# Kernel tuning notes

Measured on AMD Instinct MI355X. Metric: run time of the kernel, lower is better.

Reference implementation:

```python
import jax, jax.numpy as jnp
import numpy as np

JITTER = 1e-6
ND = 20       # num_draws
STEPS = 10    # num_steps
G = 100       # num_gammas: PG truncation terms
NUM_CLASSES = 2


def _rbf(X, outputscale, lengthscale):
    x2 = jnp.sum(X * X, axis=-1)
    d2 = jnp.maximum(x2[:, None] + x2[None, :] - 2.0 * (X @ X.T), 0.0)
    return outputscale * jnp.exp(-0.5 * d2 / (lengthscale * lengthscale))


def _chol(K):
    return jnp.linalg.cholesky(K + JITTER * jnp.eye(K.shape[-1], dtype=K.dtype))


def _pg_draw(key, c):
    # PG(1, c) via truncated infinite gamma convolution (G terms):
    # omega = (1/(2 pi^2)) * sum_k Exp(1) / ((k-1/2)^2 + c^2/(4 pi^2))
    ks = jnp.arange(1, G + 1, dtype=c.dtype)
    denom = (ks - 0.5) ** 2 + (c[..., None] ** 2) / (4.0 * jnp.pi ** 2)
    e = jax.random.exponential(key, c.shape + (G,), dtype=c.dtype)
    return jnp.sum(e / denom, axis=-1) / (2.0 * jnp.pi ** 2)


def reference(X, Y, outputscale, lengthscale):
    N = X.shape[0]
    os_ = outputscale[0]
    ls = lengthscale[0]
    K = _rbf(X, os_, ls)                          # [N,N]
    Kinv = jnp.linalg.inv(K + JITTER * jnp.eye(N, dtype=X.dtype))
    L = _chol(K)
    mu = jnp.zeros((N,), X.dtype)                 # zero mean GP
    Kinv_mu = Kinv @ mu
    y_oh = 1.0 - jax.nn.one_hot(Y, NUM_CLASSES, dtype=X.dtype)
    kappa = y_oh[:, 0] - 0.5                      # binary => 1 stick, N_sb = 1

    key = jax.random.key(42)
    k_init, k_om0, k_loop = jax.random.split(key, 3)

    # initial Gibbs state: f ~ N(mu, K) per draw
    eps0 = jax.random.normal(k_init, (ND, N), X.dtype)
    f = mu[None, :] + jnp.einsum('ij,dj->di', L, eps0)
    omega = jax.lax.stop_gradient(_pg_draw(k_om0, jax.lax.stop_gradient(f)))

    def body(state, kk):
        omega_c, f_c = state
        k1, k2 = jax.random.split(kk)
        A = Kinv[None] + jax.vmap(jnp.diag)(omega_c)         # [ND,N,N]
        sigma = jnp.linalg.inv(A)
        mu_t = jnp.einsum('dij,j->di', sigma, kappa + Kinv_mu)
        Lt = _chol(sigma)
        eps = jax.random.normal(k1, (ND, N), X.dtype)
        f_new = mu_t + jnp.einsum('dij,dj->di', Lt, eps)
        omega_new = jax.lax.stop_gradient(_pg_draw(k2, jax.lax.stop_gradient(f_new)))
        return (omega_new, f_new), None

    (omega, f), _ = jax.lax.scan(body, (omega, f), jax.random.split(k_loop, STEPS))

    # marginal log likelihood given omega (PG draws are constants)
    om = jnp.clip(omega, 1e-16)                  # [ND,N]
    Sigma_z = K[None] + jax.vmap(jnp.diag)(1.0 / om)
    Lz = _chol(Sigma_z)
    z = kappa[None, :] / om
    diff = z - mu[None, :]
    sol = jax.scipy.linalg.solve_triangular(Lz, diff[..., None], lower=True)[..., 0]
    quad = jnp.sum(sol * sol, axis=-1)
    logdet = jnp.sum(jnp.log(jnp.diagonal(Lz, axis1=-2, axis2=-1)), axis=-1)
    log2pi = float(np.log(2.0 * np.pi))
    logp = -0.5 * quad - logdet - 0.5 * N * log2pi
    mll = (logp + 0.5 * N * log2pi
           - 0.5 * jnp.sum(jnp.log(om), axis=-1)
           + 0.5 * jnp.sum(kappa[None, :] ** 2 / om, axis=-1)
           - N * float(np.log(2.0)))
    nmll = -jnp.mean(mll)
    return nmll / N


def setup_inputs() -> dict:
    key = jax.random.key(0)
    kx, ky, ko, kl = jax.random.split(key, 4)
    X = jax.random.normal(kx, (1024, 64), jnp.float32)
    Y = jax.random.randint(ky, (1024,), 0, 2)
    outputscale = jax.random.uniform(ko, (1,), jnp.float32) + 0.5
    # rescale lengthscale to ~sqrt(d) so exp(-d2/2ls^2) doesn't underflow
    lengthscale = (jax.random.uniform(kl, (1,), jnp.float32) + 0.5) * 8.0
    return {"X": X, "Y": Y, "outputscale": outputscale, "lengthscale": lengthscale}
```

## Files before the change

kernel.cpp:

```cpp
#include <hip/hip_runtime.h>
#include <stdint.h>

#define NPTS 1024
#define NDRAWS 20
#define NSTEPS 10
#define NG 100
#define PARTITIONABLE 1

#define TRI(i) (((i) * ((i) + 1)) / 2)
#define NTRI 136
#define AST ((size_t)NTRI * 4096)

typedef unsigned int u32;

__host__ __device__ static inline void tf2x32(u32 k0, u32 k1, u32 x0, u32 x1, u32* o0, u32* o1){
  u32 ks2 = k0 ^ k1 ^ 0x1BD11BDAu;
  x0 += k0; x1 += k1;
#define TFR(r) { x0 += x1; x1 = (x1 << r) | (x1 >> (32 - r)); x1 ^= x0; }
  TFR(13) TFR(15) TFR(26) TFR(6)
  x0 += k1; x1 += ks2 + 1u;
  TFR(17) TFR(29) TFR(16) TFR(24)
  x0 += ks2; x1 += k0 + 2u;
  TFR(13) TFR(15) TFR(26) TFR(6)
  x0 += k0; x1 += k1 + 3u;
// ... 221 lines not shown
#pragma unroll
    for (int a = 0; a < 4; ++a) av[a] = Pa[ty * 4 + a][k];
#pragma unroll
    for (int b = 0; b < 4; ++b) bv[b] = Pb[tx * 4 + b][k];
#pragma unroll
    for (int a = 0; a < 4; ++a)
#pragma unroll
      for (int b = 0; b < 4; ++b) acc[a][b] += av[a] * bv[b];
  }
#pragma unroll
  for (int a = 0; a < 4; ++a)
#pragma unroll
    for (int b = 0; b < 4; ++b){
      int gi = bi + ty * 4 + a, gj = bj + tx * 4 + b;
      M[(size_t)gi * NPTS + gj] -= acc[a][b];
    }
}

static void run_chol_d(double* A, double* Dinv, hipStream_t s){
  for (int p = 0; p < 16; ++p){
    k_chol_diag_inv_d<<<dim3(1), 256, 0, s>>>(A, Dinv, p);
    int nrb = 15 - p;
    if (nrb > 0){
      k_chol_panel_d<<<dim3(nrb), 256, 0, s>>>(A, Dinv, p);
      k_chol_update_d<<<dim3(nrb * (nrb + 1) / 2), 256, 0, s>>>(A, p * 64);
    }
  }
}

__global__ __launch_bounds__(256) void k_trinv_copy_diag(const double* DinvD, double* Td){
  int p = blockIdx.x;
  for (int idx = threadIdx.x; idx < 4096; idx += 256){
    int r = idx >> 6, c = idx & 63;
    Td[(size_t)(p * 64 + r) * NPTS + p * 64 + c] = DinvD[(size_t)p * 4096 + idx];
  }
}

__global__ __launch_bounds__(256) void k_trinv_part(const double* Lm, const double* Td,
                                                    double* Gs, int lev){
  int J = blockIdx.x, s = blockIdx.y;
  int I = J + lev, K = J + s;
  __shared__ double Ta[64][65];
  __shared__ double Tb[64][65];
  int tid = threadIdx.x, tx = tid & 15, ty = tid >> 4;
  for (int idx = tid; idx < 4096; idx += 256){
    int r = idx >> 6, c = idx & 63;
    Ta[r][c] = Lm[(size_t)(I * 64 + r) * NPTS + K * 64 + c];
    Tb[r][c] = Td[(size_t)(K * 64 + r) * NPTS + J * 64 + c];
  }
  __syncthreads();
  double acc[4][4];
#pragma unroll
  for (int a = 0; a < 4; ++a)
#pragma unroll
    for (int b = 0; b < 4; ++b) acc[a][b] = 0.0;
  for (int k = 0; k < 64; ++k){
    double av[4], bv[4];
#pragma unroll
    for (int a = 0; a < 4; ++a) av[a] = Ta[ty * 4 + a][k];
#pragma unroll
    for (int b = 0; b < 4; ++b) bv[b] = Tb[k][tx * 4 + b];
#pragma unroll
    for (int a = 0; a < 4; ++a)
#pragma unroll
      for (int b = 0; b < 4; ++b) acc[a][b] += av[a] * bv[b];
  }
  double* out = Gs + ((size_t)J * 15 + s) * 4096;
#pragma unroll
  for (int a = 0; a < 4; ++a)
#pragma unroll
    for (int b = 0; b < 4; ++b)
      out[(ty * 4 + a) * 64 + tx * 4 + b] = acc[a][b];
}

__global__ __launch_bounds__(256) void k_trinv_fin(double* Td, const double* Gs, int lev){
  int J = blockIdx.x, I = J + lev;
  __shared__ double Ta[64][65];
  __shared__ double Tb[64][65];
  int tid = threadIdx.x, tx = tid & 15, ty = tid >> 4;
  for (int idx = tid; idx < 4096; idx += 256){
    int r = idx >> 6, c = idx & 63;
    double g = 0.0;
    for (int s = 0; s < lev; ++s) g += Gs[((size_t)J * 15 + s) * 4096 + idx];
    Tb[r][c] = g;
    Ta[r][c] = Td[(size_t)(I * 64 + r) * NPTS + I * 64 + c];
  }
  __syncthreads();
  double ac2[4][4];
#pragma unroll
  for (int a = 0; a < 4; ++a)
#pragma unroll
    for (int b = 0; b < 4; ++b) ac2[a][b] = 0.0;
  for (int k = 0; k < 64; ++k){
    double av[4], bv[4];
#pragma unroll
    for (int a = 0; a < 4; ++a) av[a] = Ta[ty * 4 + a][k];
#pragma unroll
    for (int b = 0; b < 4; ++b) bv[b] = Tb[k][tx * 4 + b];
#pragma unroll
    for (int a = 0; a < 4; ++a)
#pragma unroll
      for (int b = 0; b < 4; ++b) ac2[a][b] += av[a] * bv[b];
  }
#pragma unroll
  for (int a = 0; a < 4; ++a)
#pragma unroll
    for (int b = 0; b < 4; ++b)
      Td[(size_t)(I * 64 + ty * 4 + a) * NPTS + J * 64 + tx * 4 + b] = -ac2[a][b];
}

__global__ __launch_bounds__(256) void k_syrk_kinv_flip(const double* Td, float* Kinvp){
  int a0, b0; tri_decode(blockIdx.x, a0, b0);
  int ti = b0, tj = a0;
  int kmin = tj;
  __shared__ double Ta[64][65];
  __shared__ double Tb[64][65];
  int tid = threadIdx.x, tx = tid & 15, ty = tid >> 4;
  double acc[4][4];
#pragma unroll
  for (int a = 0; a < 4; ++a)
#pragma unroll
    for (int b = 0; b < 4; ++b) acc[a][b] = 0.0;
  for (int K = kmin; K < 16; ++K){
    __syncthreads();
    for (int idx = tid; idx < 4096; idx += 256){
      int r = idx >> 6, c = idx & 63;
      Ta[r][c] = Td[(size_t)(K * 64 + r) * NPTS + ti * 64 + c];
      Tb[r][c] = Td[(size_t)(K * 64 + r) * NPTS + tj * 64 + c];
    }
    __syncthreads();
    for (int k = 0; k < 64; ++k){
      double av[4], bv[4];
#pragma unroll
      for (int a = 0; a < 4; ++a) av[a] = Ta[k][ty * 4 + a];
#pragma unroll
      for (int b = 0; b < 4; ++b) bv[b] = Tb[k][tx * 4 + b];
#pragma unroll
      for (int a = 0; a < 4; ++a)
#pragma unroll
        for (int b = 0; b < 4; ++b) acc[a][b] += av[a] * bv[b];
    }
  }
  int tileR = 15 - ti, tileC = 15 - tj;
  float* out = Kinvp + (size_t)(TRI(tileR) + tileC) * 4096;
#pragma unroll
  for (int a = 0; a < 4; ++a)
#pragma unroll
    for (int b = 0; b < 4; ++b){
      int rin = 63 - (ty * 4 + a), cin = 63 - (tx * 4 + b);
      out[rin * 64 + cin] = (float)acc[a][b];
    }
}

__global__ __launch_bounds__(256) void k_buildA(const float* Kinvp, const float* omega, float* Ab,
                                                int c0, int clip){
  int d = c0 + blockIdx.y;
  float* A = Ab + (size_t)blockIdx.y * AST;
  int idx4 = blockIdx.x * 256 + threadIdx.x;
  float4 v = ((const float4*)Kinvp)[idx4];
  int tile = idx4 >> 10;
  int ti, tj; tri_decode(tile, ti, tj);
  if (ti == tj){
    int e = (idx4 & 1023) * 4;
    int r = e >> 6, c = e & 63;
    if (c <= r && r < c + 4){
      float om = omega[(size_t)d * NPTS + (NPTS - 1 - (ti * 64 + r))];
      if (clip) om = fmaxf(om, 1e-16f);
      ((float*)&v)[r - c] += om;
    }
  }
  ((float4*)A)[idx4] = v;
}

__global__ __launch_bounds__(256) void k_diag0(float* Ab, float* Dinv){
  float* M = Ab + (size_t)blockIdx.x * AST;
  float* DI = Dinv + (size_t)blockIdx.x * 16 * 4096;
  __shared__ float t[64][65];
  __shared__ float Xs[64][65];
  __shared__ float diagL[64];
  int tid = threadIdx.x;
  for (int idx = tid; idx < 1024; idx += 256){
    float4 v = ((const float4*)M)[idx];
    int e = idx * 4, r = e >> 6, c = e & 63;
    t[r][c] = v.x; t[r][c + 1] = v.y; t[r][c + 2] = v.z; t[r][c + 3] = v.w;
  }
  __syncthreads();
  chol_inv_64t<float, 65>(&t[0][0], &Xs[0][0], &diagL[0], tid);
  for (int idx = tid; idx < 1024; idx += 256){
    int e = idx * 4, r = e >> 6, c = e & 63;
    float4 v, w;
    v.x = (c     <= r) ? t[r][c]     : 0.f;
    v.y = (c + 1 <= r) ? t[r][c + 1] : 0.f;
    v.z = (c + 2 <= r) ? t[r][c + 2] : 0.f;
    v.w = (c + 3 <= r) ? t[r][c + 3] : 0.f;
    w.x = Xs[r][c]; w.y = Xs[r][c + 1]; w.z = Xs[r][c + 2]; w.w = Xs[r][c + 3];
    ((float4*)M)[idx] = v;
    ((float4*)DI)[idx] = w;
  }
}

__global__ __launch_bounds__(256) void k_panel(float* Ab, const float* Dinv, int p){
  float* M = Ab + (size_t)blockIdx.y * AST;
  const float* DI = Dinv + ((size_t)blockIdx.y * 16 + p) * 4096;
  int rt = p + 1 + blockIdx.x;
  float* R = M + (size_t)(TRI(rt) + p) * 4096;
  __shared__ __align__(16) float Rst[64 * 68];
  __shared__ __align__(16) float Dst[64 * 68];
  int tid = threadIdx.x;
  for (int idx = tid; idx < 1024; idx += 256){
    float4 v = ((const float4*)R)[idx];
    float4 w = ((const float4*)DI)[idx];
    int e = idx * 4, r = e >> 6, c = e & 63;
    Rst[(c + 0) * 68 + r] = v.x; Rst[(c + 1) * 68 + r] = v.y;
    Rst[(c + 2) * 68 + r] = v.z; Rst[(c + 3) * 68 + r] = v.w;
    Dst[(c + 0) * 68 + r] = w.x; Dst[(c + 1) * 68 + r] = w.y;
    Dst[(c + 2) * 68 + r] = w.z; Dst[(c + 3) * 68 + r] = w.w;
  }
  __syncthreads();
  int tx = tid & 15, ty = tid >> 4;
  float acc[4][4];
#pragma unroll
  for (int a = 0; a < 4; ++a)
#pragma unroll
    for (int b = 0; b < 4; ++b) acc[a][b] = 0.f;
  for (int k = 0; k < 64; ++k){
    float4 av4 = *(const float4*)&Rst[k * 68 + ty * 4];
    float4 bv4 = *(const float4*)&Dst[k * 68 + tx * 4];
    float av[4] = {av4.x, av4.y, av4.z, av4.w};
    float bv[4] = {bv4.x, bv4.y, bv4.z, bv4.w};
#pragma unroll
    for (int a = 0; a < 4; ++a)
#pragma unroll
      for (int b = 0; b < 4; ++b) acc[a][b] += av[a] * bv[b];
  }
#pragma unroll
  for (int a = 0; a < 4; ++a){
    float4 v;
    v.x = acc[a][0]; v.y = acc[a][1]; v.z = acc[a][2]; v.w = acc[a][3];
    *((float4*)&R[(size_t)(ty * 4 + a) * 64 + tx * 4]) = v;
  }
}

__global__ __launch_bounds__(256) void k_update_diag(float* Ab, float* Dinv, int p){
  float* M = Ab + (size_t)blockIdx.y * AST;
  __shared__ __align__(16) float Pat[64 * 68];
  __shared__ __align__(16) float Pbt[64 * 68];
  __shared__ float diagL[64];
  int t0, t1; tri_decode(blockIdx.x, t0, t1);
  int bi = p + 1 + t0, bj = p + 1 + t1;
  const float* La = M + (size_t)(TRI(bi) + p) * 4096;
  const float* Lb = M + (size_t)(TRI(bj) + p) * 4096;
  float* Atile = M + (size_t)(TRI(bi) + bj) * 4096;
  int tid = threadIdx.x;
  for (int idx = tid; idx < 1024; idx += 256){
    float4 v = ((const float4*)La)[idx];
    float4 w = ((const float4*)Lb)[idx];
    int e = idx * 4, r = e >> 6, c = e & 63;
    Pat[(c + 0) * 68 + r] = v.x; Pat[(c + 1) * 68 + r] = v.y;
    Pat[(c + 2) * 68 + r] = v.z; Pat[(c + 3) * 68 + r] = v.w;
    Pbt[(c + 0) * 68 + r] = w.x; Pbt[(c + 1) * 68 + r] = w.y;
    Pbt[(c + 2) * 68 + r] = w.z; Pbt[(c + 3) * 68 + r] = w.w;
  }
  __syncthreads();
  int tx = tid & 15, ty = tid >> 4;
  float acc[4][4];
#pragma unroll
  for (int a = 0; a < 4; ++a)
#pragma unroll
    for (int b = 0; b < 4; ++b) acc[a][b] = 0.f;
  for (int k = 0; k < 64; ++k){
    float4 av4 = *(const float4*)&Pat[k * 68 + ty * 4];
    float4 bv4 = *(const float4*)&Pbt[k * 68 + tx * 4];
    float av[4] = {av4.x, av4.y, av4.z, av4.w};
    float bv[4] = {bv4.x, bv4.y, bv4.z, bv4.w};
#pragma unroll
    for (int a = 0; a < 4; ++a)
#pragma unroll
      for (int b = 0; b < 4; ++b) acc[a][b] += av[a] * bv[b];
  }
  if (blockIdx.x == 0){
    __syncthreads();
    for (int idx = tid; idx < 1024; idx += 256){
      float4 v = ((const float4*)Atile)[idx];
      int e = idx * 4, r = e >> 6, c = e & 63;
      Pat[r * 68 + c] = v.x; Pat[r * 68 + c + 1] = v.y;
      Pat[r * 68 + c + 2] = v.z; Pat[r * 68 + c + 3] = v.w;
    }
    __syncthreads();
#pragma unroll
    for (int a = 0; a < 4; ++a)
#pragma unroll
      for (int b = 0; b < 4; ++b)
        Pat[(ty * 4 + a) * 68 + tx * 4 + b] -= acc[a][b];
    __syncthreads();
    chol_inv_64t<float, 68>(Pat, Pbt, &diagL[0], tid);
    float* DI = Dinv + ((size_t)blockIdx.y * 16 + (p + 1)) * 4096;
    for (int idx = tid; idx < 1024; idx += 256){
      int e = idx * 4, r = e >> 6, c = e & 63;
      float4 v, w;
      v.x = (c     <= r) ? Pat[r * 68 + c]     : 0.f;
      v.y = (c + 1 <= r) ? Pat[r * 68 + c + 1] : 0.f;
      v.z = (c + 2 <= r) ? Pat[r * 68 + c + 2] : 0.f;
      v.w = (c + 3 <= r) ? Pat[r * 68 + c + 3] : 0.f;
      w.x = Pbt[r * 68 + c]; w.y = Pbt[r * 68 + c + 1];
      w.z = Pbt[r * 68 + c + 2]; w.w = Pbt[r * 68 + c + 3];
      ((float4*)Atile)[idx] = v;
      ((float4*)DI)[idx] = w;
    }
  } else {
#pragma unroll
    for (int a = 0; a < 4; ++a){
      float4 v = *((const float4*)&Atile[(size_t)(ty * 4 + a) * 64 + tx * 4]);
      v.x -= acc[a][0]; v.y -= acc[a][1]; v.z -= acc[a][2]; v.w -= acc[a][3];
      *((float4*)&Atile[(size_t)(ty * 4 + a) * 64 + tx * 4]) = v;
    }
  }
}

static void run_chol_f(float* A, float* Dinv, int batch, hipStream_t s){
  k_diag0<<<dim3(batch), 256, 0, s>>>(A, Dinv);
  for (int p = 0; p < 15; ++p){
    int nrb = 15 - p;
    k_panel<<<dim3(nrb, batch), 256, 0, s>>>(A, Dinv, p);
    k_update_diag<<<dim3(nrb * (nrb + 1) / 2, batch), 256, 0, s>>>(A, Dinv, p);
  }
}

__global__ __launch_bounds__(256) void k_step_solve(const float* Ab, const float* DinvF,
                                                    const float* kappaf, const float* eps,
                                                    float* fbuf, int c0){
  int d0 = blockIdx.x, d = c0 + d0;
  const float* L = Ab + (size_t)d0 * AST;
  const float* DI = DinvF + (size_t)d0 * 16 * 4096;
  __shared__ float z1[NPTS], z2[NPTS];
  __shared__ float buf[2][64 * 65];
  __shared__ float p1[4][64], p2[4][64];
  int tid = threadIdx.x;
  float4 rg[4];
  auto loadDI = [&](int p){
#pragma unroll
    for (int j = 0; j < 4; ++j)
      rg[j] = *(const float4*)&DI[p * 4096 + j * 1024 + tid * 4];
  };
  auto loadL = [&](int row, int col){
    const float* T = L + (size_t)(TRI(row) + col) * 4096;
#pragma unroll
    for (int j = 0; j < 4; ++j)
      rg[j] = *(const float4*)&T[j * 1024 + tid * 4];
  };
  auto store = [&](int cur){
#pragma unroll
    for (int j = 0; j < 4; ++j){
      int e = j * 1024 + tid * 4; int r = e >> 6, c = e & 63;
      float* b = &buf[cur][r * 65 + c];
      b[0] = rg[j].x; b[1] = rg[j].y; b[2] = rg[j].z; b[3] = rg[j].w;
    }
  };
  for (int i = tid; i < NPTS; i += 256){
    z1[i] = kappaf[i];
    z2[NPTS - 1 - i] = eps[(size_t)d * NPTS + i];
  }
  loadDI(0);
  int cur = 0;
  for (int p = 0; p < 16; ++p){
    for (int rb = p; rb < 16; ++rb){
      store(cur);
      int np = p, nrb = rb + 1;
      if (nrb >= 16){ np = p + 1; nrb = np; }
      if (np < 16){ if (nrb == np) loadDI(np); else loadL(nrb, np); }
      __syncthreads();
      int rr = tid & 63, q = tid >> 6;
      float s = 0.f;
#pragma unroll
      for (int cc = 0; cc < 16; ++cc)
        s += buf[cur][rr * 65 + q * 16 + cc] * z1[p * 64 + q * 16 + cc];
      p1[q][rr] = s;
      __syncthreads();
      if (tid < 64){
        float v = p1[0][tid] + p1[1][tid] + p1[2][tid] + p1[3][tid];
        if (rb == p) z1[p * 64 + tid] = v;
        else z1[rb * 64 + tid] -= v;
      }
      __syncthreads();
      cur ^= 1;
    }
  }
  loadDI(15);
  for (int p = 15; p >= 0; --p){
    for (int cb = p; cb >= 0; --cb){
      store(cur);
      int np = p, ncb = cb - 1;
      if (ncb < 0){ np = p - 1; ncb = np; }
      if (np >= 0){ if (ncb == np) loadDI(np); else loadL(np, ncb); }
      __syncthreads();
      int cc = tid & 63, q = tid >> 6;
      float s1 = 0.f, s2 = 0.f;
#pragma unroll
      for (int rr = 0; rr < 16; ++rr){
        float t = buf[cur][(q * 16 + rr) * 65 + cc];
        s1 += t * z1[p * 64 + q * 16 + rr];
        s2 += t * z2[p * 64 + q * 16 + rr];
      }
      p1[q][cc] = s1; p2[q][cc] = s2;
      __syncthreads();
      if (tid < 64){
        float v1 = p1[0][tid] + p1[1][tid] + p1[2][tid] + p1[3][tid];
        float v2 = p2[0][tid] + p2[1][tid] + p2[2][tid] + p2[3][tid];
        if (cb == p){ z1[p * 64 + tid] = v1; z2[p * 64 + tid] = v2; }
        else { z1[cb * 64 + tid] -= v1; z2[cb * 64 + tid] -= v2; }
      }
      __syncthreads();
      cur ^= 1;
    }
  }
  for (int i = tid; i < NPTS; i += 256)
    fbuf[(size_t)d * NPTS + i] = z1[NPTS - 1 - i] + z2[NPTS - 1 - i];
}

__global__ __launch_bounds__(256) void k_final3(const float* Ab, const float* DinvF,
                                                const float* kappaf, const float* ldetK,
                                                float* mll, int c0){
  int d0 = blockIdx.x, d = c0 + d0;
  const float* L = Ab + (size_t)d0 * AST;
  const float* DI = DinvF + (size_t)d0 * 16 * 4096;
  __shared__ float z[NPTS];
  __shared__ float buf[2][64 * 65];
  __shared__ float part[4][64];
  __shared__ float redq[4];
  int tid = threadIdx.x;
  float4 rg[4];
  auto loadDI = [&](int p){
#pragma unroll
    for (int j = 0; j < 4; ++j)
      rg[j] = *(const float4*)&DI[p * 4096 + j * 1024 + tid * 4];
  };
  auto loadL = [&](int rbrow, int pcol){
    const float* T = L + (size_t)(TRI(rbrow) + pcol) * 4096;
#pragma unroll
    for (int j = 0; j < 4; ++j)
      rg[j] = *(const float4*)&T[j * 1024 + tid * 4];
  };
  auto store = [&](int cur){
#pragma unroll
    for (int j = 0; j < 4; ++j){
      int e = j * 1024 + tid * 4; int r = e >> 6, c = e & 63;
      float* b = &buf[cur][r * 65 + c];
      b[0] = rg[j].x; b[1] = rg[j].y; b[2] = rg[j].z; b[3] = rg[j].w;
    }
  };
  for (int i = tid; i < NPTS; i += 256) z[i] = kappaf[i];
  loadDI(0);
  int cur = 0;
  float ldacc = 0.f;
  for (int p = 0; p < 16; ++p){
    for (int rb = p; rb < 16; ++rb){
      store(cur);
      int np = p, nrb = rb + 1;
      if (nrb >= 16){ np = p + 1; nrb = np; }
      if (np < 16){ if (nrb == np) loadDI(np); else loadL(nrb, np); }
      __syncthreads();
      if (rb == p && tid < 64) ldacc += logf(buf[cur][tid * 65 + tid]);
      int rr = tid & 63, q = tid >> 6;
      float s = 0.f;
#pragma unroll
      for (int cc = 0; cc < 16; ++cc)
        s += buf[cur][rr * 65 + q * 16 + cc] * z[p * 64 + q * 16 + cc];
      part[q][rr] = s;
      __syncthreads();
      if (tid < 64){
        float v = part[0][tid] + part[1][tid] + part[2][tid] + part[3][tid];
        if (rb == p) z[p * 64 + tid] = v;
        else z[rb * 64 + tid] -= v;
      }
      __syncthreads();
      cur ^= 1;
    }
  }
  float q2 = 0.f;
  for (int i = tid; i < NPTS; i += 256) q2 += z[i] * z[i];
  int wid = tid >> 6, lane = tid & 63;
  for (int o = 32; o; o >>= 1) q2 += __shfl_down(q2, o);
  if (lane == 0) redq[wid] = q2;
  __syncthreads();
  if (tid < 64){
    float ldv = ldacc;
    for (int o = 32; o; o >>= 1) ldv += __shfl_down(ldv, o);
    if (tid == 0){
      float q2t = redq[0] + redq[1] + redq[2] + redq[3];
      mll[d] = 0.5f * q2t + ldv - 0.5f * ldetK[0] - 709.7827128933839f;
    }
  }
}

__global__ __launch_bounds__(256) void k_gen_eps(u32 ka, u32 kb, float* eps){
  int i = blockIdx.x * 256 + threadIdx.x;
  if (i >= NDRAWS * NPTS) return;
  u32 bits = rand32(ka, kb, (u32)i, (u32)(NDRAWS * NPTS));
  eps[i] = normal_from_bits(bits);
}

__global__ __launch_bounds__(256) void k_init_f2(const float* Lf, const float* eps, float* f){
  int d = blockIdx.y, rb = blockIdx.x;
  __shared__ float tile[64][65];
  __shared__ float ev[64];
  __shared__ float part[4][64];
  int tid = threadIdx.x;
  int r = tid & 63, q = tid >> 6;
  float acc = 0.f;
  for (int kt = 0; kt <= rb; ++kt){
    __syncthreads();
#pragma unroll
    for (int j = 0; j < 4; ++j){
      int e = j * 1024 + tid * 4; int rr = e >> 6, cc = e & 63;
      float4 v = *(const float4*)&Lf[(size_t)(rb * 64 + rr) * NPTS + kt * 64 + cc];
      tile[rr][cc] = v.x; tile[rr][cc + 1] = v.y; tile[rr][cc + 2] = v.z; tile[rr][cc + 3] = v.w;
    }
    if (tid < 64) ev[tid] = eps[(size_t)d * NPTS + kt * 64 + tid];
    __syncthreads();
    int cmax = (kt == rb) ? (r + 1) : 64;
    for (int cc = q * 16; cc < q * 16 + 16; ++cc){
      if (cc < cmax) acc += tile[r][cc] * ev[cc];
    }
  }
  part[q][r] = acc;
  __syncthreads();
  if (tid < 64){
    float s = part[0][tid] + part[1][tid] + part[2][tid] + part[3][tid];
    f[(size_t)d * NPTS + rb * 64 + tid] = s;
  }
}

__global__ __launch_bounds__(256) void k_pg(u32 ka, u32 kb, const float* f, float* omega){
  int idx = blockIdx.x * 256 + threadIdx.x;
  if (idx >= NDRAWS * NPTS) return;
  float c = f[idx];
  float c2w = (c * c) / 39.47841760435743f;
  float sum = 0.f;
  u32 base = (u32)idx * NG;
  for (int g = 0; g < NG; ++g){
    u32 bits = rand32(ka, kb, base + (u32)g, (u32)(NDRAWS * NPTS * NG));
    float u = u01f(bits);
    float e = -log1pf(-u);
    float kk = (float)g + 0.5f;
    sum += e / (kk * kk + c2w);
  }
  omega[idx] = sum / 19.739208802178716f;
}

__global__ void k_out(const float* mll, float* out){
  if (threadIdx.x == 0){
    float s = 0.f;
    for (int dd = 0; dd < NDRAWS; ++dd) s += mll[dd];
    float m = s / (float)NDRAWS;
    out[0] = (-m) / (float)NPTS;
  }
}

static void host_split(u32 ka, u32 kb, int num, u32* outA, u32* outB){
#if PARTITIONABLE
  for (int j = 0; j < num; ++j) tf2x32(ka, kb, 0u, (u32)j, &outA[j], &outB[j]);
#else
  u32 flat[40];
  for (int k = 0; k < num; ++k){
    u32 a, b; tf2x32(ka, kb, (u32)k, (u32)(num + k), &a, &b);
    flat[k] = a; flat[num + k] = b;
  }
  for (int j = 0; j < num; ++j){ outA[j] = flat[2 * j]; outB[j] = flat[2 * j + 1]; }
#endif
}

extern "C" void kernel_launch(void* const* d_in, const int* in_sizes, int n_in,
                              void* d_out, int out_size, void* d_ws, size_t ws_size,
                              hipStream_t stream){
  const float* X  = (const float*)d_in[0];
  const int*   Y  = (const int*)d_in[1];
  const float* osp = (const float*)d_in[2];
  const float* lsp = (const float*)d_in[3];
  float* out = (float*)d_out;

  const size_t NN = (size_t)NPTS * NPTS;
  char* p = (char*)d_ws;
  float* Kinvp  = (float*)p;  p += AST * 4;
  float* omega  = (float*)p;  p += (size_t)NDRAWS * NPTS * 4;
  float* fbuf   = (float*)p;  p += (size_t)NDRAWS * NPTS * 4;
  float* epsb   = (float*)p;  p += (size_t)NDRAWS * NPTS * 4;
  float* kappaf = (float*)p;  p += NPTS * 4;
  float* x2     = (float*)p;  p += NPTS * 4;
  float* mll    = (float*)p;  p += 128;
  float* ldetK  = (float*)p;  p += 128;
  uintptr_t ip = (uintptr_t)p; ip = (ip + 255) & ~(uintptr_t)255;
  char* cb = (char*)ip;

  double* Ld    = (double*)cb;
  double* Td    = (double*)(cb + NN * 8);
  double* DinvD = (double*)(cb + NN * 16);
  float*  Lf    = (float*)(cb + NN * 16 + (size_t)16 * 4096 * 8);
  double* Gslc  = (double*)(cb + NN * 16 + (size_t)16 * 4096 * 8 + NN * 4);

  size_t rem = ws_size - (size_t)(cb - (char*)d_ws);
  const size_t PER_DRAW = AST * 4 + (size_t)16 * 4096 * 4;
  int CH = (int)(rem / PER_DRAW);
  if (CH > NDRAWS) CH = NDRAWS;
  if (CH < 1) CH = 1;
  float* bufA  = (float*)cb;
  float* dinvF = (float*)(cb + (size_t)CH * AST * 4);

  u32 r3A[3], r3B[3];
  host_split(0u, 42u, 3, r3A, r3B);
  u32 kiA = r3A[0], kiB = r3B[0];
  u32 koA = r3A[1], koB = r3B[1];
  u32 klA = r3A[2], klB = r3B[2];
  u32 kkA[NSTEPS], kkB[NSTEPS];
  host_split(klA, klB, NSTEPS, kkA, kkB);
  u32 k1A[NSTEPS], k1B[NSTEPS], k2A[NSTEPS], k2B[NSTEPS];
  for (int t = 0; t < NSTEPS; ++t){
    u32 sA[2], sB[2];
    host_split(kkA[t], kkB[t], 2, sA, sB);
    k1A[t] = sA[0]; k1B[t] = sB[0];
    k2A[t] = sA[1]; k2B[t] = sB[1];
  }

  k_prep<<<dim3(4), 256, 0, stream>>>(X, Y, x2, kappaf);
  k_computeK<<<dim3(64, 64), dim3(16, 16), 0, stream>>>(X, x2, osp, lsp, Ld);
  run_chol_d(Ld, DinvD, stream);
  k_castL<<<dim3(4096), 256, 0, stream>>>(Ld, Lf);
  k_logdetK<<<dim3(1), 256, 0, stream>>>(Ld, ldetK);
  k_trinv_copy_diag<<<dim3(16), 256, 0, stream>>>(DinvD, Td);
  for (int lev = 1; lev < 16; ++lev){
    k_trinv_part<<<dim3(16 - lev, lev), 256, 0, stream>>>(Ld, Td, Gslc, lev);
    k_trinv_fin<<<dim3(16 - lev), 256, 0, stream>>>(Td, Gslc, lev);
  }
  k_syrk_kinv_flip<<<dim3(NTRI), 256, 0, stream>>>(Td, Kinvp);

  k_gen_eps<<<dim3(80), 256, 0, stream>>>(kiA, kiB, epsb);
  k_init_f2<<<dim3(16, NDRAWS), 256, 0, stream>>>(Lf, epsb, fbuf);
  k_pg<<<dim3(80), 256, 0, stream>>>(koA, koB, fbuf, omega);

  for (int t = 0; t < NSTEPS; ++t){
    k_gen_eps<<<dim3(80), 256, 0, stream>>>(k1A[t], k1B[t], epsb);
    for (int c0 = 0; c0 < NDRAWS; c0 += CH){
      int nb = NDRAWS - c0 < CH ? NDRAWS - c0 : CH;
      k_buildA<<<dim3(544, nb), 256, 0, stream>>>(Kinvp, omega, bufA, c0, 0);
      run_chol_f(bufA, dinvF, nb, stream);
      k_step_solve<<<dim3(nb), 256, 0, stream>>>(bufA, dinvF, kappaf, epsb, fbuf, c0);
    }
    k_pg<<<dim3(80), 256, 0, stream>>>(k2A[t], k2B[t], fbuf, omega);
  }

  for (int c0 = 0; c0 < NDRAWS; c0 += CH){
    int nb = NDRAWS - c0 < CH ? NDRAWS - c0 : CH;
    k_buildA<<<dim3(544, nb), 256, 0, stream>>>(Kinvp, omega, bufA, c0, 1);
    run_chol_f(bufA, dinvF, nb, stream);
    k_final3<<<dim3(nb), 256, 0, stream>>>(bufA, dinvF, kappaf, ldetK, mll, c0);
  }
  k_out<<<dim3(1), 64, 0, stream>>>(mll, out);
}
```

Baseline: 23.16 ms.

## Fuse panel solve into trailing update via S=D^T D and fold eps/PG into stage kernels

Restructures the blocked Cholesky of each draw's precision matrix. The panel kernel is removed: L panels are never formed explicitly. Instead the trailing update uses A_ip * S_p * A_jp^T, where S_p = Dinv^T Dinv is precomputed per diagonal block, which halves the number of launches per panel step. The solve kernels are adapted to work with unscaled A panels through an intermediate y vector. Eps generation is folded into the build stage and the Polya-Gamma draw into the solve kernel, which removes separate launches. The trade-off is extra workspace for S, a second small GEMM inside every update block, and extra FLOPs, with some numerical risk from forming Dinv^T Dinv.

Result: slower. 26.47 ms (+14.3%).

```diff
diff --git a/kernel.cpp b/kernel.cpp
--- a/kernel.cpp
+++ b/kernel.cpp
@@ -397,198 +397,237 @@
     }
 }
 
-__global__ __launch_bounds__(256) void k_buildA(const float* Kinvp, const float* omega, float* Ab,
-                                                int c0, int clip){
-  int d = c0 + blockIdx.y;
-  float* A = Ab + (size_t)blockIdx.y * AST;
-  int idx4 = blockIdx.x * 256 + threadIdx.x;
-  float4 v = ((const float4*)Kinvp)[idx4];
-  int tile = idx4 >> 10;
-  int ti, tj; tri_decode(tile, ti, tj);
-  if (ti == tj){
-    int e = (idx4 & 1023) * 4;
-    int r = e >> 6, c = e & 63;
-    if (c <= r && r < c + 4){
-      float om = omega[(size_t)d * NPTS + (NPTS - 1 - (ti * 64 + r))];
+
+__global__ __launch_bounds__(256) void k_stage0(const float* Kinvp, const float* omega,
+    float* Ab, float* DinvF, float* Sbuf, float* epsb,
+    int c0, int nb, int clip, int doeps, u32 ka, u32 kb){
+  int nA = 544 * nb;
+  int task = blockIdx.x, tid = threadIdx.x;
+  if (task < nA){
+    int dd = task / 544, blk = task - dd * 544;
+    int d = c0 + dd;
+    float* A = Ab + (size_t)dd * AST;
+    int idx4 = blk * 256 + tid;
+    float4 v = ((const float4*)Kinvp)[idx4];
+    int tile = idx4 >> 10;
+    int ti, tj; tri_decode(tile, ti, tj);
+    if (ti == tj){
+      int e = (idx4 & 1023) * 4;
+      int r = e >> 6, c = e & 63;
+      if (c <= r && r < c + 4){
+        float om = omega[(size_t)d * NPTS + (NPTS - 1 - (ti * 64 + r))];
+        if (clip) om = fmaxf(om, 1e-16f);
+        ((float*)&v)[r - c] += om;
+      }
+    }
+    ((float4*)A)[idx4] = v;
+  } else if (task < nA + nb){
+    int dd = task - nA, d = c0 + dd;
+    __shared__ float t[64 * 65];
+    __shared__ float Xs[64 * 65];
+    __shared__ float diagL[64];
+    for (int idx = tid; idx < 1024; idx += 256){
+      float4 v = ((const float4*)Kinvp)[idx];
+      int e = idx * 4, r = e >> 6, c = e & 63;
+      t[r * 65 + c] = v.x; t[r * 65 + c + 1] = v.y;
+      t[r * 65 + c + 2] = v.z; t[r * 65 + c + 3] = v.w;
+    }
+    __syncthreads();
+    if (tid < 64){
+      float om = omega[(size_t)d * NPTS + (NPTS - 1 - tid)];
       if (clip) om = fmaxf(om, 1e-16f);
-      ((float*)&v)[r - c] += om;
-    }
-  }
-  ((float4*)A)[idx4] = v;
-}
-
-__global__ __launch_bounds__(256) void k_diag0(float* Ab, float* Dinv){
-  float* M = Ab + (size_t)blockIdx.x * AST;
-  float* DI = Dinv + (size_t)blockIdx.x * 16 * 4096;
-  __shared__ float t[64][65];
-  __shared__ float Xs[64][65];
+      t[tid * 65 + tid] += om;
+    }
+    __syncthreads();
+    chol_inv_64t<float, 65>(t, Xs, diagL, tid);
+    float* DI = DinvF + (size_t)dd * 16 * 4096;
+    for (int idx = tid; idx < 1024; idx += 256){
+      int e = idx * 4, r = e >> 6, c = e & 63;
+      float4 w;
+      w.x = Xs[r * 65 + c]; w.y = Xs[r * 65 + c + 1];
+      w.z = Xs[r * 65 + c + 2]; w.w = Xs[r * 65 + c + 3];
+      ((float4*)DI)[idx] = w;
+    }
+    int tx = tid & 15, ty = tid >> 4;
+    float sa[4][4];
+#pragma unroll
+    for (int a = 0; a < 4; ++a)
+#pragma unroll
+      for (int b = 0; b < 4; ++b) sa[a][b] = 0.f;
+    for (int m = 0; m < 64; ++m){
+      float av[4], bv[4];
+#pragma unroll
+      for (int a = 0; a < 4; ++a) av[a] = Xs[m * 65 + ty * 4 + a];
+#pragma unroll
+      for (int b = 0; b < 4; ++b) bv[b] = Xs[m * 65 + tx * 4 + b];
+#pragma unroll
+      for (int a = 0; a < 4; ++a)
+#pragma unroll
+        for (int b = 0; b < 4; ++b) sa[a][b] += av[a] * bv[b];
+    }
+    float* So = Sbuf + (size_t)dd * 16 * 4096;
+#pragma unroll
+    for (int a = 0; a < 4; ++a)
+#pragma unroll
+      for (int b = 0; b < 4; ++b)
+        So[(ty * 4 + a) * 64 + tx * 4 + b] = sa[a][b];
+  } else if (doeps){
+    int i = (task - nA - nb) * 256 + tid;
+    if (i < nb * NPTS){
+      int g = c0 * NPTS + i;
+      u32 bits = rand32(ka, kb, (u32)g, (u32)(NDRAWS * NPTS));
+      epsb[g] = normal_from_bits(bits);
+    }
+  }
+}
+
+__global__ __launch_bounds__(256) void k_updstage(float* Ab, float* DinvF, float* Sbuf,
+                                                  int p, int npairs){
+  int task = blockIdx.x, tid = threadIdx.x;
+  int dd = task / npairs, pr = task - dd * npairs;
+  int t0, t1; tri_decode(pr, t0, t1);
+  int bi = p + 1 + t0, bj = p + 1 + t1;
+  float* M = Ab + (size_t)dd * AST;
+  const float* Sp = Sbuf + ((size_t)dd * 16 + p) * 4096;
+  __shared__ float A1[64 * 65];
+  __shared__ float A2[64 * 65];
+  __shared__ float Xb[64 * 65];
   __shared__ float diagL[64];
-  int tid = threadIdx.x;
+  int tx = tid & 15, ty = tid >> 4;
+  const float* Abi = M + (size_t)(TRI(bi) + p) * 4096;
   for (int idx = tid; idx < 1024; idx += 256){
-    float4 v = ((const float4*)M)[idx];
+    float4 v = ((const float4*)Abi)[idx];
+    float4 w = ((const float4*)Sp)[idx];
     int e = idx * 4, r = e >> 6, c = e & 63;
-    t[r][c] = v.x; t[r][c + 1] = v.y; t[r][c + 2] = v.z; t[r][c + 3] = v.w;
-  }
-  __syncthreads();
-  chol_inv_64t<float, 65>(&t[0][0], &Xs[0][0], &diagL[0], tid);
-  for (int idx = tid; idx < 1024; idx += 256){
-    int e = idx * 4, r = e >> 6, c = e & 63;
-    float4 v, w;
-    v.x = (c     <= r) ? t[r][c]     : 0.f;
-    v.y = (c + 1 <= r) ? t[r][c + 1] : 0.f;
-    v.z = (c + 2 <= r) ? t[r][c + 2] : 0.f;
-    v.w = (c + 3 <= r) ? t[r][c + 3] : 0.f;
-    w.x = Xs[r][c]; w.y = Xs[r][c + 1]; w.z = Xs[r][c + 2]; w.w = Xs[r][c + 3];
-    ((float4*)M)[idx] = v;
-    ((float4*)DI)[idx] = w;
-  }
-}
-
-__global__ __launch_bounds__(256) void k_panel(float* Ab, const float* Dinv, int p){
-  float* M = Ab + (size_t)blockIdx.y * AST;
-  const float* DI = Dinv + ((size_t)blockIdx.y * 16 + p) * 4096;
-  int rt = p + 1 + blockIdx.x;
-  float* R = M + (size_t)(TRI(rt) + p) * 4096;
-  __shared__ __align__(16) float Rst[64 * 68];
-  __shared__ __align__(16) float Dst[64 * 68];
-  int tid = threadIdx.x;
-  for (int idx = tid; idx < 1024; idx += 256){
-    float4 v = ((const float4*)R)[idx];
-    float4 w = ((const float4*)DI)[idx];
-    int e = idx * 4, r = e >> 6, c = e & 63;
-    Rst[(c + 0) * 68 + r] = v.x; Rst[(c + 1) * 68 + r] = v.y;
-    Rst[(c + 2) * 68 + r] = v.z; Rst[(c + 3) * 68 + r] = v.w;
-    Dst[(c + 0) * 68 + r] = w.x; Dst[(c + 1) * 68 + r] = w.y;
-    Dst[(c + 2) * 68 + r] = w.z; Dst[(c + 3) * 68 + r] = w.w;
-  }
-  __syncthreads();
-  int tx = tid & 15, ty = tid >> 4;
+    A1[r * 65 + c] = v.x; A1[r * 65 + c + 1] = v.y;
+    A1[r * 65 + c + 2] = v.z; A1[r * 65 + c + 3] = v.w;
+    Xb[r * 65 + c] = w.x; Xb[r * 65 + c + 1] = w.y;
+    Xb[r * 65 + c + 2] = w.z; Xb[r * 65 + c + 3] = w.w;
+  }
+  if (bi != bj){
+    const float* Abj = M + (size_t)(TRI(bj) + p) * 4096;
+    for (int idx = tid; idx < 1024; idx += 256){
+      float4 v = ((const float4*)Abj)[idx];
+      int e = idx * 4, r = e >> 6, c = e & 63;
+      A2[r * 65 + c] = v.x; A2[r * 65 + c + 1] = v.y;
+      A2[r * 65 + c + 2] = v.z; A2[r * 65 + c + 3] = v.w;
+    }
+  }
+  __syncthreads();
   float acc[4][4];
 #pragma unroll
   for (int a = 0; a < 4; ++a)
 #pragma unroll
     for (int b = 0; b < 4; ++b) acc[a][b] = 0.f;
+  for (int m = 0; m < 64; ++m){
+    float av[4], bv[4];
+#pragma unroll
+    for (int a = 0; a < 4; ++a) av[a] = A1[(ty * 4 + a) * 65 + m];
+#pragma unroll
+    for (int b = 0; b < 4; ++b) bv[b] = Xb[m * 65 + tx * 4 + b];
+#pragma unroll
+    for (int a = 0; a < 4; ++a)
+#pragma unroll
+      for (int b = 0; b < 4; ++b) acc[a][b] += av[a] * bv[b];
+  }
+  __syncthreads();
+#pragma unroll
+  for (int a = 0; a < 4; ++a)
+#pragma unroll
+    for (int b = 0; b < 4; ++b)
+      Xb[(ty * 4 + a) * 65 + tx * 4 + b] = acc[a][b];
+  __syncthreads();
+  const float* A2p = (bi == bj) ? A1 : A2;
+  float ac2[4][4];
+#pragma unroll
+  for (int a = 0; a < 4; ++a)
+#pragma unroll
+    for (int b = 0; b < 4; ++b) ac2[a][b] = 0.f;
   for (int k = 0; k < 64; ++k){
-    float4 av4 = *(const float4*)&Rst[k * 68 + ty * 4];
-    float4 bv4 = *(const float4*)&Dst[k * 68 + tx * 4];
-    float av[4] = {av4.x, av4.y, av4.z, av4.w};
-    float bv[4] = {bv4.x, bv4.y, bv4.z, bv4.w};
+    float av[4], bv[4];
+#pragma unroll
+    for (int a = 0; a < 4; ++a) av[a] = Xb[(ty * 4 + a) * 65 + k];
+#pragma unroll
+    for (int b = 0; b < 4; ++b) bv[b] = A2p[(tx * 4 + b) * 65 + k];
 #pragma unroll
     for (int a = 0; a < 4; ++a)
 #pragma unroll
-      for (int b = 0; b < 4; ++b) acc[a][b] += av[a] * bv[b];
-  }
-#pragma unroll
-  for (int a = 0; a < 4; ++a){
-    float4 v;
-    v.x = acc[a][0]; v.y = acc[a][1]; v.z = acc[a][2]; v.w = acc[a][3];
-    *((float4*)&R[(size_t)(ty * 4 + a) * 64 + tx * 4]) = v;
-  }
-}
-
-__global__ __launch_bounds__(256) void k_update_diag(float* Ab, float* Dinv, int p){
-  float* M = Ab + (size_t)blockIdx.y * AST;
-  __shared__ __align__(16) float Pat[64 * 68];
-  __shared__ __align__(16) float Pbt[64 * 68];
-  __shared__ float diagL[64];
-  int t0, t1; tri_decode(blockIdx.x, t0, t1);
-  int bi = p + 1 + t0, bj = p + 1 + t1;
-  const float* La = M + (size_t)(TRI(bi) + p) * 4096;
-  const float* Lb = M + (size_t)(TRI(bj) + p) * 4096;
+      for (int b = 0; b < 4; ++b) ac2[a][b] += av[a] * bv[b];
+  }
   float* Atile = M + (size_t)(TRI(bi) + bj) * 4096;
-  int tid = threadIdx.x;
-  for (int idx = tid; idx < 1024; idx += 256){
-    float4 v = ((const float4*)La)[idx];
-    float4 w = ((const float4*)Lb)[idx];
-    int e = idx * 4, r = e >> 6, c = e & 63;
-    Pat[(c + 0) * 68 + r] = v.x; Pat[(c + 1) * 68 + r] = v.y;
-    Pat[(c + 2) * 68 + r] = v.z; Pat[(c + 3) * 68 + r] = v.w;
-    Pbt[(c + 0) * 68 + r] = w.x; Pbt[(c + 1) * 68 + r] = w.y;
-    Pbt[(c + 2) * 68 + r] = w.z; Pbt[(c + 3) * 68 + r] = w.w;
-  }
-  __syncthreads();
-  int tx = tid & 15, ty = tid >> 4;
-  float acc[4][4];
-#pragma unroll
-  for (int a = 0; a < 4; ++a)
-#pragma unroll
-    for (int b = 0; b < 4; ++b) acc[a][b] = 0.f;
-  for (int k = 0; k < 64; ++k){
-    float4 av4 = *(const float4*)&Pat[k * 68 + ty * 4];
-    float4 bv4 = *(const float4*)&Pbt[k * 68 + tx * 4];
-    float av[4] = {av4.x, av4.y, av4.z, av4.w};
-    float bv[4] = {bv4.x, bv4.y, bv4.z, bv4.w};
-#pragma unroll
-    for (int a = 0; a < 4; ++a)
-#pragma unroll
-      for (int b = 0; b < 4; ++b) acc[a][b] += av[a] * bv[b];
-  }
-  if (blockIdx.x == 0){
+  if (!(t0 == 0 && t1 == 0)){
+#pragma unroll
+    for (int a = 0; a < 4; ++a){
+      float4 v = *((const float4*)&Atile[(size_t)(ty * 4 + a) * 64 + tx * 4]);
+      v.x -= ac2[a][0]; v.y -= ac2[a][1]; v.z -= ac2[a][2]; v.w -= ac2[a][3];
+      *((float4*)&Atile[(size_t)(ty * 4 + a) * 64 + tx * 4]) = v;
+    }
+  } else {
     __syncthreads();
     for (int idx = tid; idx < 1024; idx += 256){
       float4 v = ((const float4*)Atile)[idx];
       int e = idx * 4, r = e >> 6, c = e & 63;
-      Pat[r * 68 + c] = v.x; Pat[r * 68 + c + 1] = v.y;
-      Pat[r * 68 + c + 2] = v.z; Pat[r * 68 + c + 3] = v.w;
+      A1[r * 65 + c] = v.x; A1[r * 65 + c + 1] = v.y;
+      A1[r * 65 + c + 2] = v.z; A1[r * 65 + c + 3] = v.w;
     }
     __syncthreads();
 #pragma unroll
     for (int a = 0; a < 4; ++a)
 #pragma unroll
       for (int b = 0; b < 4; ++b)
-        Pat[(ty * 4 + a) * 68 + tx * 4 + b] -= acc[a][b];
+        A1[(ty * 4 + a) * 65 + tx * 4 + b] -= ac2[a][b];
     __syncthreads();
-    chol_inv_64t<float, 68>(Pat, Pbt, &diagL[0], tid);
-    float* DI = Dinv + ((size_t)blockIdx.y * 16 + (p + 1)) * 4096;
+    chol_inv_64t<float, 65>(A1, A2, diagL, tid);
+    float* DI = DinvF + ((size_t)dd * 16 + (p + 1)) * 4096;
     for (int idx = tid; idx < 1024; idx += 256){
       int e = idx * 4, r = e >> 6, c = e & 63;
-      float4 v, w;
-      v.x = (c     <= r) ? Pat[r * 68 + c]     : 0.f;
-      v.y = (c + 1 <= r) ? Pat[r * 68 + c + 1] : 0.f;
-      v.z = (c + 2 <= r) ? Pat[r * 68 + c + 2] : 0.f;
-      v.w = (c + 3 <= r) ? Pat[r * 68 + c + 3] : 0.f;
-      w.x = Pbt[r * 68 + c]; w.y = Pbt[r * 68 + c + 1];
-      w.z = Pbt[r * 68 + c + 2]; w.w = Pbt[r * 68 + c + 3];
-      ((float4*)Atile)[idx] = v;
+      float4 w;
+      w.x = A2[r * 65 + c]; w.y = A2[r * 65 + c + 1];
+      w.z = A2[r * 65 + c + 2]; w.w = A2[r * 65 + c + 3];
       ((float4*)DI)[idx] = w;
     }
-  } else {
-#pragma unroll
-    for (int a = 0; a < 4; ++a){
-      float4 v = *((const float4*)&Atile[(size_t)(ty * 4 + a) * 64 + tx * 4]);
-      v.x -= acc[a][0]; v.y -= acc[a][1]; v.z -= acc[a][2]; v.w -= acc[a][3];
-      *((float4*)&Atile[(size_t)(ty * 4 + a) * 64 + tx * 4]) = v;
-    }
-  }
-}
-
-static void run_chol_f(float* A, float* Dinv, int batch, hipStream_t s){
-  k_diag0<<<dim3(batch), 256, 0, s>>>(A, Dinv);
-  for (int p = 0; p < 15; ++p){
-    int nrb = 15 - p;
-    k_panel<<<dim3(nrb, batch), 256, 0, s>>>(A, Dinv, p);
-    k_update_diag<<<dim3(nrb * (nrb + 1) / 2, batch), 256, 0, s>>>(A, Dinv, p);
-  }
-}
-
-__global__ __launch_bounds__(256) void k_step_solve(const float* Ab, const float* DinvF,
-                                                    const float* kappaf, const float* eps,
-                                                    float* fbuf, int c0){
-  int d0 = blockIdx.x, d = c0 + d0;
-  const float* L = Ab + (size_t)d0 * AST;
-  const float* DI = DinvF + (size_t)d0 * 16 * 4096;
-  __shared__ float z1[NPTS], z2[NPTS];
+    float sa[4][4];
+#pragma unroll
+    for (int a = 0; a < 4; ++a)
+#pragma unroll
+      for (int b = 0; b < 4; ++b) sa[a][b] = 0.f;
+    for (int m = 0; m < 64; ++m){
+      float av[4], bv[4];
+#pragma unroll
+      for (int a = 0; a < 4; ++a) av[a] = A2[m * 65 + ty * 4 + a];
+#pragma unroll
+      for (int b = 0; b < 4; ++b) bv[b] = A2[m * 65 + tx * 4 + b];
+#pragma unroll
+      for (int a = 0; a < 4; ++a)
+#pragma unroll
+        for (int b = 0; b < 4; ++b) sa[a][b] += av[a] * bv[b];
+    }
+    float* So = Sbuf + ((size_t)dd * 16 + (p + 1)) * 4096;
+#pragma unroll
+    for (int a = 0; a < 4; ++a)
+#pragma unroll
+      for (int b = 0; b < 4; ++b)
+        So[(ty * 4 + a) * 64 + tx * 4 + b] = sa[a][b];
+  }
+}
+
+__global__ __launch_bounds__(256) void k_solve_pg(const float* Ab, const float* DinvF,
+    const float* kappaf, const float* eps, float* omega, int c0, u32 ka, u32 kb){
+  int dd = blockIdx.x, d = c0 + dd;
+  const float* M = Ab + (size_t)dd * AST;
+  const float* DIb = DinvF + (size_t)dd * 16 * 4096;
+  __shared__ float z1[1024], z2[1024], u1[1024], u2[1024], y[64];
   __shared__ float buf[2][64 * 65];
-  __shared__ float p1[4][64], p2[4][64];
+  __shared__ float p1[256], p2[256];
   int tid = threadIdx.x;
   float4 rg[4];
   auto loadDI = [&](int p){
 #pragma unroll
     for (int j = 0; j < 4; ++j)
-      rg[j] = *(const float4*)&DI[p * 4096 + j * 1024 + tid * 4];
+      rg[j] = *(const float4*)&DIb[p * 4096 + j * 1024 + tid * 4];
   };
-  auto loadL = [&](int row, int col){
-    const float* T = L + (size_t)(TRI(row) + col) * 4096;
+  auto loadA = [&](int row, int col){
+    const float* T = M + (size_t)(TRI(row) + col) * 4096;
 #pragma unroll
     for (int j = 0; j < 4; ++j)
       rg[j] = *(const float4*)&T[j * 1024 + tid * 4];
@@ -604,6 +643,7 @@
   for (int i = tid; i < NPTS; i += 256){
     z1[i] = kappaf[i];
     z2[NPTS - 1 - i] = eps[(size_t)d * NPTS + i];
+    u1[i] = 0.f; u2[i] = 0.f;
   }
   loadDI(0);
   int cur = 0;
@@ -612,21 +652,36 @@
       store(cur);
       int np = p, nrb = rb + 1;
       if (nrb >= 16){ np = p + 1; nrb = np; }
-      if (np < 16){ if (nrb == np) loadDI(np); else loadL(nrb, np); }
+      if (np < 16){ if (nrb == np) loadDI(np); else loadA(nrb, np); }
       __syncthreads();
       int rr = tid & 63, q = tid >> 6;
-      float s = 0.f;
-#pragma unroll
-      for (int cc = 0; cc < 16; ++cc)
-        s += buf[cur][rr * 65 + q * 16 + cc] * z1[p * 64 + q * 16 + cc];
-      p1[q][rr] = s;
-      __syncthreads();
-      if (tid < 64){
-        float v = p1[0][tid] + p1[1][tid] + p1[2][tid] + p1[3][tid];
-        if (rb == p) z1[p * 64 + tid] = v;
-        else z1[rb * 64 + tid] -= v;
+      if (rb == p){
+        float s = 0.f;
+#pragma unroll
+        for (int cc = 0; cc < 16; ++cc)
+          s += buf[cur][rr * 65 + q * 16 + cc] * z1[p * 64 + q * 16 + cc];
+        p1[q * 64 + rr] = s;
+        __syncthreads();
+        if (tid < 64) z1[p * 64 + tid] = p1[tid] + p1[64 + tid] + p1[128 + tid] + p1[192 + tid];
+        __syncthreads();
+        float s2 = 0.f;
+#pragma unroll
+        for (int r2 = 0; r2 < 16; ++r2)
+          s2 += buf[cur][(q * 16 + r2) * 65 + rr] * z1[p * 64 + q * 16 + r2];
+        p1[q * 64 + rr] = s2;
+        __syncthreads();
+        if (tid < 64) y[tid] = p1[tid] + p1[64 + tid] + p1[128 + tid] + p1[192 + tid];
+        __syncthreads();
+      } else {
+        float s = 0.f;
+#pragma unroll
+        for (int cc = 0; cc < 16; ++cc)
+          s += buf[cur][rr * 65 + q * 16 + cc] * y[q * 16 + cc];
+        p1[q * 64 + rr] = s;
+        __syncthreads();
+        if (tid < 64) z1[rb * 64 + tid] -= p1[tid] + p1[64 + tid] + p1[128 + tid] + p1[192 + tid];
+        __syncthreads();
       }
-      __syncthreads();
       cur ^= 1;
     }
   }
@@ -636,51 +691,91 @@
       store(cur);
       int np = p, ncb = cb - 1;
       if (ncb < 0){ np = p - 1; ncb = np; }
-      if (np >= 0){ if (ncb == np) loadDI(np); else loadL(np, ncb); }
+      if (np >= 0){ if (ncb == np) loadDI(np); else loadA(np, ncb); }
       __syncthreads();
-      int cc = tid & 63, q = tid >> 6;
-      float s1 = 0.f, s2 = 0.f;
-#pragma unroll
-      for (int rr = 0; rr < 16; ++rr){
-        float t = buf[cur][(q * 16 + rr) * 65 + cc];
-        s1 += t * z1[p * 64 + q * 16 + rr];
-        s2 += t * z2[p * 64 + q * 16 + rr];
+      int rr = tid & 63, q = tid >> 6;
+      if (cb == p){
+        float s1 = 0.f, s2 = 0.f;
+#pragma unroll
+        for (int cc = 0; cc < 16; ++cc){
+          float t = buf[cur][rr * 65 + q * 16 + cc];
+          s1 += t * u1[p * 64 + q * 16 + cc];
+          s2 += t * u2[p * 64 + q * 16 + cc];
+        }
+        p1[q * 64 + rr] = s1; p2[q * 64 + rr] = s2;
+        __syncthreads();
+        if (tid < 64){
+          z1[p * 64 + tid] -= p1[tid] + p1[64 + tid] + p1[128 + tid] + p1[192 + tid];
+          z2[p * 64 + tid] -= p2[tid] + p2[64 + tid] + p2[128 + tid] + p2[192 + tid];
+        }
+        __syncthreads();
+        s1 = 0.f; s2 = 0.f;
+#pragma unroll
+        for (int r2 = 0; r2 < 16; ++r2){
+          float t = buf[cur][(q * 16 + r2) * 65 + rr];
+          s1 += t * z1[p * 64 + q * 16 + r2];
+          s2 += t * z2[p * 64 + q * 16 + r2];
+        }
+        p1[q * 64 + rr] = s1; p2[q * 64 + rr] = s2;
+        __syncthreads();
+        if (tid < 64){
+          z1[p * 64 + tid] = p1[tid] + p1[64 + tid] + p1[128 + tid] + p1[192 + tid];
+          z2[p * 64 + tid] = p2[tid] + p2[64 + tid] + p2[128 + tid] + p2[192 + tid];
+        }
+        __syncthreads();
+      } else {
+        float s1 = 0.f, s2 = 0.f;
+#pragma unroll
+        for (int r2 = 0; r2 < 16; ++r2){
+          float t = buf[cur][(q * 16 + r2) * 65 + rr];
+          s1 += t * z1[p * 64 + q * 16 + r2];
+          s2 += t * z2[p * 64 + q * 16 + r2];
+        }
+        p1[q * 64 + rr] = s1; p2[q * 64 + rr] = s2;
+        __syncthreads();
+        if (tid < 64){
+          u1[cb * 64 + tid] += p1[tid] + p1[64 + tid] + p1[128 + tid] + p1[192 + tid];
+          u2[cb * 64 + tid] += p2[tid] + p2[64 + tid] + p2[128 + tid] + p2[192 + tid];
+        }
+        __syncthreads();
       }
-      p1[q][cc] = s1; p2[q][cc] = s2;
-      __syncthreads();
-      if (tid < 64){
-        float v1 = p1[0][tid] + p1[1][tid] + p1[2][tid] + p1[3][tid];
-        float v2 = p2[0][tid] + p2[1][tid] + p2[2][tid] + p2[3][tid];
-        if (cb == p){ z1[p * 64 + tid] = v1; z2[p * 64 + tid] = v2; }
-        else { z1[cb * 64 + tid] -= v1; z2[cb * 64 + tid] -= v2; }
-      }
-      __syncthreads();
       cur ^= 1;
     }
   }
-  for (int i = tid; i < NPTS; i += 256)
-    fbuf[(size_t)d * NPTS + i] = z1[NPTS - 1 - i] + z2[NPTS - 1 - i];
-}
-
-__global__ __launch_bounds__(256) void k_final3(const float* Ab, const float* DinvF,
-                                                const float* kappaf, const float* ldetK,
-                                                float* mll, int c0){
-  int d0 = blockIdx.x, d = c0 + d0;
-  const float* L = Ab + (size_t)d0 * AST;
-  const float* DI = DinvF + (size_t)d0 * 16 * 4096;
-  __shared__ float z[NPTS];
+  for (int i = tid; i < NPTS; i += 256){
+    float c = z1[NPTS - 1 - i] + z2[NPTS - 1 - i];
+    float c2w = (c * c) / 39.47841760435743f;
+    float sum = 0.f;
+    u32 base = (u32)((size_t)d * NPTS + i) * NG;
+    for (int g = 0; g < NG; ++g){
+      u32 bits = rand32(ka, kb, base + (u32)g, (u32)(NDRAWS * NPTS * NG));
+      float u = u01f(bits);
+      float e = -log1pf(-u);
+      float kk = (float)g + 0.5f;
+      sum += e / (kk * kk + c2w);
+    }
+    omega[(size_t)d * NPTS + i] = sum / 19.739208802178716f;
+  }
+}
+
+__global__ __launch_bounds__(256) void k_final_w(const float* Ab, const float* DinvF,
+    const float* kappaf, const float* ldetK, float* mll, int c0){
+  int dd = blockIdx.x, d = c0 + dd;
+  const float* M = Ab + (size_t)dd * AST;
+  const float* DIb = DinvF + (size_t)dd * 16 * 4096;
+  __shared__ float z1[1024], y[64];
   __shared__ float buf[2][64 * 65];
-  __shared__ float part[4][64];
+  __shared__ float p1[256];
   __shared__ float redq[4];
   int tid = threadIdx.x;
   float4 rg[4];
   auto loadDI = [&](int p){
 #pragma unroll
     for (int j = 0; j < 4; ++j)
-      rg[j] = *(const float4*)&DI[p * 4096 + j * 1024 + tid * 4];
+      rg[j] = *(const float4*)&DIb[p * 4096 + j * 1024 + tid * 4];
   };
-  auto loadL = [&](int rbrow, int pcol){
-    const float* T = L + (size_t)(TRI(rbrow) + pcol) * 4096;
+  auto loadA = [&](int row, int col){
+    const float* T = M + (size_t)(TRI(row) + col) * 4096;
 #pragma unroll
     for (int j = 0; j < 4; ++j)
       rg[j] = *(const float4*)&T[j * 1024 + tid * 4];
@@ -693,7 +788,7 @@
       b[0] = rg[j].x; b[1] = rg[j].y; b[2] = rg[j].z; b[3] = rg[j].w;
     }
   };
-  for (int i = tid; i < NPTS; i += 256) z[i] = kappaf[i];
+  for (int i = tid; i < NPTS; i += 256) z1[i] = kappaf[i];
   loadDI(0);
   int cur = 0;
   float ldacc = 0.f;
@@ -702,27 +797,42 @@
       store(cur);
       int np = p, nrb = rb + 1;
       if (nrb >= 16){ np = p + 1; nrb = np; }
-      if (np < 16){ if (nrb == np) loadDI(np); else loadL(nrb, np); }
+      if (np < 16){ if (nrb == np) loadDI(np); else loadA(nrb, np); }
       __syncthreads();
-      if (rb == p && tid < 64) ldacc += logf(buf[cur][tid * 65 + tid]);
       int rr = tid & 63, q = tid >> 6;
-      float s = 0.f;
-#pragma unroll
-      for (int cc = 0; cc < 16; ++cc)
-        s += buf[cur][rr * 65 + q * 16 + cc] * z[p * 64 + q * 16 + cc];
-      part[q][rr] = s;
-      __syncthreads();
-      if (tid < 64){
-        float v = part[0][tid] + part[1][tid] + part[2][tid] + part[3][tid];
-        if (rb == p) z[p * 64 + tid] = v;
-        else z[rb * 64 + tid] -= v;
+      if (rb == p){
+        if (tid < 64) ldacc += logf(buf[cur][tid * 65 + tid]);
+        float s = 0.f;
+#pragma unroll
+        for (int cc = 0; cc < 16; ++cc)
+          s += buf[cur][rr * 65 + q * 16 + cc] * z1[p * 64 + q * 16 + cc];
+        p1[q * 64 + rr] = s;
+        __syncthreads();
+        if (tid < 64) z1[p * 64 + tid] = p1[tid] + p1[64 + tid] + p1[128 + tid] + p1[192 + tid];
+        __syncthreads();
+        float s2 = 0.f;
+#pragma unroll
+        for (int r2 = 0; r2 < 16; ++r2)
+          s2 += buf[cur][(q * 16 + r2) * 65 + rr] * z1[p * 64 + q * 16 + r2];
+        p1[q * 64 + rr] = s2;
+        __syncthreads();
+        if (tid < 64) y[tid] = p1[tid] + p1[64 + tid] + p1[128 + tid] + p1[192 + tid];
+        __syncthreads();
+      } else {
+        float s = 0.f;
+#pragma unroll
+        for (int cc = 0; cc < 16; ++cc)
+          s += buf[cur][rr * 65 + q * 16 + cc] * y[q * 16 + cc];
+        p1[q * 64 + rr] = s;
+        __syncthreads();
+        if (tid < 64) z1[rb * 64 + tid] -= p1[tid] + p1[64 + tid] + p1[128 + tid] + p1[192 + tid];
+        __syncthreads();
       }
-      __syncthreads();
       cur ^= 1;
     }
   }
   float q2 = 0.f;
-  for (int i = tid; i < NPTS; i += 256) q2 += z[i] * z[i];
+  for (int i = tid; i < NPTS; i += 256) q2 += z1[i] * z1[i];
   int wid = tid >> 6, lane = tid & 63;
   for (int o = 32; o; o >>= 1) q2 += __shfl_down(q2, o);
   if (lane == 0) redq[wid] = q2;
@@ -843,12 +953,13 @@
   double* Gslc  = (double*)(cb + NN * 16 + (size_t)16 * 4096 * 8 + NN * 4);
 
   size_t rem = ws_size - (size_t)(cb - (char*)d_ws);
-  const size_t PER_DRAW = AST * 4 + (size_t)16 * 4096 * 4;
+  const size_t PER_DRAW = AST * 4 + (size_t)16 * 4096 * 4 * 2;
   int CH = (int)(rem / PER_DRAW);
   if (CH > NDRAWS) CH = NDRAWS;
   if (CH < 1) CH = 1;
   float* bufA  = (float*)cb;
   float* dinvF = (float*)(cb + (size_t)CH * AST * 4);
+  float* sbuf  = (float*)(cb + (size_t)CH * (AST * 4 + (size_t)16 * 4096 * 4));
 
   u32 r3A[3], r3B[3];
   host_split(0u, 42u, 3, r3A, r3B);
@@ -882,21 +993,30 @@
   k_pg<<<dim3(80), 256, 0, stream>>>(koA, koB, fbuf, omega);
 
   for (int t = 0; t < NSTEPS; ++t){
-    k_gen_eps<<<dim3(80), 256, 0, stream>>>(k1A[t], k1B[t], epsb);
     for (int c0 = 0; c0 < NDRAWS; c0 += CH){
       int nb = NDRAWS - c0 < CH ? NDRAWS - c0 : CH;
-      k_buildA<<<dim3(544, nb), 256, 0, stream>>>(Kinvp, omega, bufA, c0, 0);
-      run_chol_f(bufA, dinvF, nb, stream);
-      k_step_solve<<<dim3(nb), 256, 0, stream>>>(bufA, dinvF, kappaf, epsb, fbuf, c0);
-    }
-    k_pg<<<dim3(80), 256, 0, stream>>>(k2A[t], k2B[t], fbuf, omega);
+      k_stage0<<<dim3(544 * nb + nb + nb * 4), 256, 0, stream>>>(
+          Kinvp, omega, bufA, dinvF, sbuf, epsb, c0, nb, 0, 1, k1A[t], k1B[t]);
+      for (int pp = 0; pp < 15; ++pp){
+        int nr = 15 - pp;
+        int npair = nr * (nr + 1) / 2;
+        k_updstage<<<dim3(npair * nb), 256, 0, stream>>>(bufA, dinvF, sbuf, pp, npair);
+      }
+      k_solve_pg<<<dim3(nb), 256, 0, stream>>>(bufA, dinvF, kappaf, epsb, omega,
+                                               c0, k2A[t], k2B[t]);
+    }
   }
 
   for (int c0 = 0; c0 < NDRAWS; c0 += CH){
     int nb = NDRAWS - c0 < CH ? NDRAWS - c0 : CH;
-    k_buildA<<<dim3(544, nb), 256, 0, stream>>>(Kinvp, omega, bufA, c0, 1);
-    run_chol_f(bufA, dinvF, nb, stream);
-    k_final3<<<dim3(nb), 256, 0, stream>>>(bufA, dinvF, kappaf, ldetK, mll, c0);
+    k_stage0<<<dim3(544 * nb + nb), 256, 0, stream>>>(
+        Kinvp, omega, bufA, dinvF, sbuf, epsb, c0, nb, 1, 0, 0u, 0u);
+    for (int pp = 0; pp < 15; ++pp){
+      int nr = 15 - pp;
+      int npair = nr * (nr + 1) / 2;
+      k_updstage<<<dim3(npair * nb), 256, 0, stream>>>(bufA, dinvF, sbuf, pp, npair);
+    }
+    k_final_w<<<dim3(nb), 256, 0, stream>>>(bufA, dinvF, kappaf, ldetK, mll, c0);
   }
   k_out<<<dim3(1), 64, 0, stream>>>(mll, out);
 }
```
